# Performance work log

Measured on AMD Instinct MI355X. Metric: run time of the kernel, lower is better.

## Reference

```python
import jax, jax.numpy as jnp
import numpy as np

B, S, D, H = 1, 2048, 768, 12
E, K, I = 8, 2, 1024          # routed experts, top-k, expert inter dim
IS = 2 * I                    # shared-expert inter dim (n_shared_experts * moe_inter_dim)
EPS = 1e-5
ROUTE_SCALE = 1.0


def rmsnorm(x, w, eps=EPS):
    xf = x.astype(jnp.float32)
    return (xf * jax.lax.rsqrt(jnp.mean(xf * xf, axis=-1, keepdims=True) + eps)).astype(x.dtype) * w


def setup_inputs() -> dict:
    key = jax.random.key(0)
    ks = jax.random.split(key, 8)
    sc = 0.02
    return {
        "x": jax.random.normal(ks[0], (B, S, D), jnp.float32),
        "norm1_w": jnp.ones((D,), jnp.float32),
        "norm3_w": jnp.ones((D,), jnp.float32),
        "gate_w": jax.random.normal(ks[1], (E, D), jnp.float32) * sc,
        "w1": jax.random.normal(ks[2], (E, I, D), jnp.float32) * sc,
        "b1": jnp.zeros((E, I), jnp.float32),
        "w2": jax.random.normal(ks[3], (E, D, I), jnp.float32) * sc,
        "b2": jnp.zeros((E, D), jnp.float32),
        "w3": jax.random.normal(ks[4], (E, I, D), jnp.float32) * sc,
        "b3": jnp.zeros((E, I), jnp.float32),
        "fc1_w": jax.random.normal(ks[5], (IS, D), jnp.float32) * sc,
        "fc1_b": jnp.zeros((IS,), jnp.float32),
        "fc2_w": jax.random.normal(ks[6], (D, IS), jnp.float32) * sc,
        "fc2_b": jnp.zeros((D,), jnp.float32),
    }


def _forward(x, norm1_w, norm3_w, gate_w, w1, b1, w2, b2, w3, b3,
             fc1_w, fc1_b, fc2_w, fc2_b):
    b, s, d = x.shape
    hd = d // H

    # ---- self-attention (no qkv/out projections in the original module) ----
    xn = rmsnorm(x, norm1_w)
    qkv = xn.reshape(b, s, H, hd).transpose(0, 2, 1, 3)      # [b,h,s,hd]
    scores = jnp.einsum("bhqd,bhkd->bhqk", qkv, qkv) / np.sqrt(hd)
    attn = jax.nn.softmax(scores, axis=-1)
    ao = jnp.einsum("bhqk,bhkd->bhqd", attn, qkv)
    attn_out = ao.transpose(0, 2, 1, 3).reshape(b, s, d)
    out = x + attn_out

    # ---- MoE on norm3(out) ----
    xf = rmsnorm(out, norm3_w).reshape(-1, d)                # [N, D]
    n = xf.shape[0]

    # Gate: softmax scoring, n_groups=1 (no group masking), no bias (dim != 7168)
    logits = xf @ gate_w.T                                    # [N, E]
    sc = jax.nn.softmax(logits.astype(jnp.float32), axis=-1)  # max-subtract folded in
    _, idx = jax.lax.top_k(sc, K)                             # [N, K]
    weights = jnp.take_along_axis(sc, idx, axis=-1)
    weights = jnp.clip(weights, 1e-7) * ROUTE_SCALE
    weights = weights.astype(xf.dtype)

    # combine matrix: per-token dense expert weights (zeros for unselected)
    cmb = jnp.zeros((n, E), xf.dtype).at[jnp.arange(n)[:, None], idx].add(weights)

    # SwiGLU experts, batched over E (zero combine weight == not dispatched)
    a = jnp.einsum("nd,eid->nei", xf, w1) + b1                # [N,E,I]
    g = jnp.einsum("nd,eid->nei", xf, w3) + b3
    h = jax.nn.silu(a) * g
    eo = jnp.einsum("nei,edi->ned", h, w2) + b2               # [N,E,D]
    y = jnp.einsum("ned,ne->nd", eo, cmb)

    # shared experts (SiLU MLP)
    z = jax.nn.silu(xf @ fc1_w.T + fc1_b) @ fc2_w.T + fc2_b

    moe_out = (y + z).reshape(b, s, d)
    return out + moe_out


def reference(x, norm1_w, norm3_w, gate_w, w1, b1, w2, b2, w3, b3,
              fc1_w, fc1_b, fc2_w, fc2_b):
    return _forward(x, norm1_w, norm3_w, gate_w, w1, b1, w2, b2, w3, b3,
                    fc1_w, fc1_b, fc2_w, fc2_b)
```

## Files before the change

### kernel.cpp

```cpp
#include <hip/hip_runtime.h>
#include <math.h>

#define SEQ    2048
#define DMODEL 768
#define NHEAD  12
#define NEXP   8
#define IDIM   1024
#define ISH    2048
#define KVS    4
#define NE2    10
#define ATTN_BLOCKS 1536
#define CVT_BLOCKS 10752

typedef unsigned short u16;
typedef short s16x8 __attribute__((ext_vector_type(8)));
typedef u16   u16x8 __attribute__((ext_vector_type(8)));
typedef float f32x4 __attribute__((ext_vector_type(4)));

#define MFMA_BF16(a, b, c) __builtin_amdgcn_mfma_f32_16x16x32_bf16((a), (b), (c), 0, 0, 0)

__device__ __forceinline__ void glds16(const void* g, void* l) {
  __builtin_amdgcn_global_load_lds(
      (const __attribute__((address_space(1))) unsigned int*)g,
      (__attribute__((address_space(3))) unsigned int*)l, 16, 0, 0);
}

__device__ __forceinline__ u16 f2b(float f) {
  unsigned int u = __float_as_uint(f);
  unsigned int r = u + 0x7fffu + ((u >> 16) & 1u);
  return (u16)(r >> 16);
}
__device__ __forceinline__ float b2f(u16 v) {
  return __uint_as_float(((unsigned int)v) << 16);
}

__global__ __launch_bounds__(256) void rmsnorm_kernel(const float* __restrict__ x,
                                                      const float* __restrict__ n1w,
                                                      u16* __restrict__ xnb,
                                                      int* __restrict__ counts) {
  const int tid = threadIdx.x;
  if (blockIdx.x == 0 && tid < 16) counts[tid] = 0;
  const int row = blockIdx.x;
  const float* r = x + (size_t)row * DMODEL;
  float v0 = r[tid], v1 = r[tid + 256], v2 = r[tid + 512];
  float ss = v0 * v0 + v1 * v1 + v2 * v2;
  __shared__ float red[256];
  red[tid] = ss;
  __syncthreads();
  for (int s = 128; s > 0; s >>= 1) {
    if (tid < s) red[tid] += red[tid + s];
    __syncthreads();
  }
  float rms = rsqrtf(red[0] * (1.f / DMODEL) + 1e-5f);
  u16* ob = xnb + (size_t)row * DMODEL;
  ob[tid]       = f2b(v0 * rms * n1w[tid]);
  ob[tid + 256] = f2b(v1 * rms * n1w[tid + 256]);
  ob[tid + 512] = f2b(v2 * rms * n1w[tid + 512]);
}

__global__ __launch_bounds__(256) void attn_cvt_kernel(
    const u16* __restrict__ xnb, u16* __restrict__ Opart,
    float* __restrict__ Mpart, float* __restrict__ Lpart,
    const float* __restrict__ w1, const float* __restrict__ w3, const float* __restrict__ w2,
    const float* __restrict__ fc1, const float* __restrict__ fc2,
    u16* __restrict__ w1b, u16* __restrict__ w3b, u16* __restrict__ w2b,
    u16* __restrict__ fc1b, u16* __restrict__ fc2b) {
  const int tid = threadIdx.x;
  if (blockIdx.x >= ATTN_BLOCKS) {
    long i = (long)(blockIdx.x - ATTN_BLOCKS) * 256 + tid;
    const long NW8 = (long)NEXP * IDIM * DMODEL / 8;
    const long NF8 = (long)ISH * DMODEL / 8;
    const float* s; u16* d; long o;
    if      (i < NW8)             { s = w1;  d = w1b;  o = i; }
    else if (i < 2 * NW8)         { s = w3;  d = w3b;  o = i - NW8; }
    else if (i < 3 * NW8)         { s = w2;  d = w2b;  o = i - 2 * NW8; }
    else if (i < 3 * NW8 + NF8)   { s = fc1; d = fc1b; o = i - 3 * NW8; }
    else                          { s = fc2; d = fc2b; o = i - 3 * NW8 - NF8; }
    float4 a = ((const float4*)s)[2 * o], b = ((const float4*)s)[2 * o + 1];
    u16x8 v;
    v[0] = f2b(a.x); v[1] = f2b(a.y); v[2] = f2b(a.z); v[3] = f2b(a.w);
    v[4] = f2b(b.x); v[5] = f2b(b.y); v[6] = f2b(b.z); v[7] = f2b(b.w);
    ((u16x8*)d)[o] = v;
    return;
  }
  __shared__ u16 Qs[64][72];
  __shared__ u16 Ks[64][72];
  __shared__ u16 Vt[64][72];
  __shared__ u16 Ps[64][72];
  const int q0 = (blockIdx.x & 31) * 64;
  const int h = (blockIdx.x >> 5) % NHEAD;
  const int kvs = blockIdx.x / (32 * NHEAD);
  const int lane = tid & 63, w = tid >> 6;
  const int quad = lane >> 4, l15 = lane & 15;
  const size_t hoff = (size_t)h * 64;

  for (int cc = tid; cc < 512; cc += 256) {
    int row = cc >> 3, col8 = (cc & 7) * 8;
    *(u16x8*)&Qs[row][col8] = *(const u16x8*)(xnb + (size_t)(q0 + row) * DMODEL + hoff + col8);
  }
  __syncthreads();
  const s16x8 aq0 = *(const s16x8*)&Qs[16 * w + l15][quad * 8];
  const s16x8 aq1 = *(const s16x8*)&Qs[16 * w + l15][32 + quad * 8];

  f32x4 o[4] = {};
  float mrow[4], lrow[4];
#pragma unroll
  for (int r = 0; r < 4; r++) { mrow[r] = -INFINITY; lrow[r] = 0.f; }

  const int it0 = kvs * (SEQ / 64 / KVS);
  for (int it = 0; it < SEQ / 64 / KVS; it++) {
    const int k0 = (it0 + it) * 64;
    for (int cc = tid; cc < 512; cc += 256) {
      int row = cc >> 3, col8 = (cc & 7) * 8;
      *(u16x8*)&Ks[row][col8] = *(const u16x8*)(xnb + (size_t)(k0 + row) * DMODEL + hoff + col8);
    }
    __syncthreads();

    {
      const int rp = tid & 31, dc = ((tid >> 5) & 7) * 8;
      u16x8 v0 = *(const u16x8*)&Ks[2 * rp][dc];
      u16x8 v1 = *(const u16x8*)&Ks[2 * rp + 1][dc];
#pragma unroll
      for (int j = 0; j < 8; j++) {
        *(unsigned int*)&Vt[dc + j][2 * rp] =
            (unsigned int)v0[j] | ((unsigned int)v1[j] << 16);
      }
    }

    f32x4 s4[4] = {};
#pragma unroll
    for (int jt = 0; jt < 4; jt++) {
      s16x8 b0 = *(const s16x8*)&Ks[16 * jt + l15][quad * 8];
      s16x8 b1 = *(const s16x8*)&Ks[16 * jt + l15][32 + quad * 8];
      s4[jt] = MFMA_BF16(aq0, b0, s4[jt]);
      s4[jt] = MFMA_BF16(aq1, b1, s4[jt]);
      s4[jt] *= 0.125f;
    }

#pragma unroll
    for (int r = 0; r < 4; r++) {
      float mx = mrow[r];
#pragma unroll
      for (int jt = 0; jt < 4; jt++) mx = fmaxf(mx, s4[jt][r]);
#pragma unroll
      for (int m = 1; m <= 8; m <<= 1) mx = fmaxf(mx, __shfl_xor(mx, m, 64));
      float al = __expf(mrow[r] - mx);
      mrow[r] = mx;
      float pv[4], sum = 0.f;
#pragma unroll
      for (int jt = 0; jt < 4; jt++) { pv[jt] = __expf(s4[jt][r] - mx); sum += pv[jt]; }
#pragma unroll
      for (int m = 1; m <= 8; m <<= 1) sum += __shfl_xor(sum, m, 64);
      lrow[r] = lrow[r] * al + sum;
#pragma unroll
      for (int jt = 0; jt < 4; jt++) o[jt][r] *= al;
#pragma unroll
      for (int jt = 0; jt < 4; jt++) Ps[16 * w + quad * 4 + r][16 * jt + l15] = f2b(pv[jt]);
    }
    __syncthreads();

    s16x8 ap0 = *(const s16x8*)&Ps[16 * w + l15][quad * 8];
    s16x8 ap1 = *(const s16x8*)&Ps[16 * w + l15][32 + quad * 8];
#pragma unroll
    for (int jt = 0; jt < 4; jt++) {
      s16x8 bv0 = *(const s16x8*)&Vt[16 * jt + l15][quad * 8];
      s16x8 bv1 = *(const s16x8*)&Vt[16 * jt + l15][32 + quad * 8];
      o[jt] = MFMA_BF16(ap0, bv0, o[jt]);
      o[jt] = MFMA_BF16(ap1, bv1, o[jt]);
    }
  }

  const int hk = h * KVS + kvs;
#pragma unroll
  for (int r = 0; r < 4; r++) {
    int q = q0 + 16 * w + quad * 4 + r;
    size_t base = (size_t)q * (KVS * NHEAD) + hk;
#pragma unroll
    for (int jt = 0; jt < 4; jt++)
      Opart[base * 64 + 16 * jt + l15] = f2b(o[jt][r]);
    if (l15 == 0) {
      Mpart[base] = mrow[r];
      Lpart[base] = lrow[r];
    }
  }
}

__global__ __launch_bounds__(256) void fused_post_kernel(
    const u16* __restrict__ Opart, const float* __restrict__ Mpart,
    const float* __restrict__ Lpart, const float* __restrict__ x,
    const float* __restrict__ n3w, const float* __restrict__ gw,
    u16* __restrict__ xfb, float* __restrict__ out,
    int* __restrict__ counts, int* __restrict__ toklist, float* __restrict__ wtlist) {
  const int t = blockIdx.x;
  const int tid = threadIdx.x;
  const int lane = tid & 63, w = tid >> 6;
  __shared__ u16 Os[48 * 64];
  __shared__ float MsLs[96];
  __shared__ float ssP[4];
  __shared__ float geP[4][NEXP];

  const u16* orow = Opart + (size_t)t * (48 * 64);
  for (int c = tid; c < 384; c += 256)
    *(u16x8*)&Os[c * 8] = *(const u16x8*)&orow[c * 8];
  if (tid < 96)
    MsLs[tid] = (tid < 48) ? Mpart[(size_t)t * 48 + tid]
                           : Lpart[(size_t)t * 48 + (tid - 48)];
  __syncthreads();

  float val[3];
  float ss = 0.f;
  const float* xr = x + (size_t)t * DMODEL;
  float* outr = out + (size_t)t * DMODEL;
#pragma unroll
  for (int j = 0; j < 3; j++) {
    const int ii = 3 * w + j;
    float m0 = MsLs[ii * 4 + 0], m1 = MsLs[ii * 4 + 1];
    float m2 = MsLs[ii * 4 + 2], m3 = MsLs[ii * 4 + 3];
    float mh = fmaxf(fmaxf(m0, m1), fmaxf(m2, m3));
    float c0 = __expf(m0 - mh), c1 = __expf(m1 - mh);
    float c2 = __expf(m2 - mh), c3 = __expf(m3 - mh);
    float Lh = c0 * MsLs[48 + ii * 4 + 0] + c1 * MsLs[48 + ii * 4 + 1] +
               c2 * MsLs[48 + ii * 4 + 2] + c3 * MsLs[48 + ii * 4 + 3];
    float O = c0 * b2f(Os[(ii * 4 + 0) * 64 + lane]) +
              c1 * b2f(Os[(ii * 4 + 1) * 64 + lane]) +
              c2 * b2f(Os[(ii * 4 + 2) * 64 + lane]) +
              c3 * b2f(Os[(ii * 4 + 3) * 64 + lane]);
    float v = xr[ii * 64 + lane] + O / Lh;
    outr[ii * 64 + lane] = v;
    val[j] = v;
    ss += v * v;
  }
#pragma unroll
  for (int off = 32; off >= 1; off >>= 1) ss += __shfl_xor(ss, off, 64);
  if (lane == 0) ssP[w] = ss;
  __syncthreads();
  float rms = rsqrtf((ssP[0] + ssP[1] + ssP[2] + ssP[3]) * (1.f / DMODEL) + 1e-5f);

  float ge[NEXP] = {};
#pragma unroll
  for (int j = 0; j < 3; j++) {
    int c = (3 * w + j) * 64 + lane;
    float xn = val[j] * rms * n3w[c];
    xfb[(size_t)t * DMODEL + c] = f2b(xn);
#pragma unroll
    for (int e = 0; e < NEXP; e++) ge[e] = fmaf(xn, gw[e * DMODEL + c], ge[e]);
  }
#pragma unroll
  for (int off = 32; off >= 1; off >>= 1)
#pragma unroll
    for (int e = 0; e < NEXP; e++) ge[e] += __shfl_xor(ge[e], off, 64);
  if (lane == 0)
#pragma unroll
    for (int e = 0; e < NEXP; e++) geP[w][e] = ge[e];
  __syncthreads();

  if (tid == 0) {
    float p[NEXP], mx = -INFINITY, s = 0.f;
#pragma unroll
    for (int e = 0; e < NEXP; e++) {
      p[e] = geP[0][e] + geP[1][e] + geP[2][e] + geP[3][e];
      mx = fmaxf(mx, p[e]);
    }
#pragma unroll
    for (int e = 0; e < NEXP; e++) { p[e] = __expf(p[e] - mx); s += p[e]; }
    int e0 = 0; float b0 = p[0];
    for (int e = 1; e < NEXP; e++) if (p[e] > b0) { b0 = p[e]; e0 = e; }
    int e1 = -1; float b1v = -1.f;
    for (int e = 0; e < NEXP; e++) if (e != e0 && p[e] > b1v) { b1v = p[e]; e1 = e; }
    float inv = 1.f / s;
    int pos0 = atomicAdd(&counts[e0], 1);
    toklist[e0 * SEQ + pos0] = t;
    wtlist[e0 * SEQ + pos0] = fmaxf(b0 * inv, 1e-7f);
    int pos1 = atomicAdd(&counts[e1], 1);
    toklist[e1 * SEQ + pos1] = t;
    wtlist[e1 * SEQ + pos1] = fmaxf(b1v * inv, 1e-7f);
  }
}

__global__ __launch_bounds__(256) void gemm1_kernel(
    const u16* __restrict__ xfb,
    const u16* __restrict__ w1b, const u16* __restrict__ w3b, const u16* __restrict__ fc1b,
    const float* __restrict__ b1, const float* __restrict__ b3, const float* __restrict__ fc1_b,
    const int* __restrict__ counts, const int* __restrict__ toklist, u16* __restrict__ hb) {
  __shared__ u16 As[64][32];
  __shared__ u16 W1s[128][32];
  __shared__ u16 W3s[128][32];
  __shared__ int rIdx[64];
  const int e = blockIdx.z;
  const bool routed = (e < NEXP);
  int cnt, off;
  if (routed) {
    cnt = counts[e];
    off = 0;
    for (int i = 0; i < e; i++) off += counts[i];
  } else {
    cnt = SEQ;
    off = 2 * SEQ + (e - NEXP) * SEQ;
  }
  const int m0 = blockIdx.y * 64;
  if (m0 >= cnt) return;
  const int n0 = blockIdx.x * 128;
  const int tid = threadIdx.x;
  if (tid < 64) {
    int rr = m0 + tid;
    rIdx[tid] = routed ? toklist[e * SEQ + (rr < cnt ? rr : cnt - 1)] : rr;
  }
  __syncthreads();
  const u16* W1 = routed ? w1b + (size_t)e * IDIM * DMODEL
                         : fc1b + (size_t)(e - NEXP) * IDIM * DMODEL;
  const ptrdiff_t d31 = w3b - w1b;

  const int lane = tid & 63, w = tid >> 6;
  const int quad = lane >> 4, l15 = lane & 15;
  const int wy = w >> 1, wx = w & 1;
  const int srow = lane >> 2;
  const int schunk = ((lane & 3) ^ ((lane >> 3) & 3)) * 8;
  const int cb = (quad ^ ((l15 >> 1) & 3)) * 8;

  const u16* aS   = xfb + (size_t)rIdx[16 * w + srow] * DMODEL + schunk;
  const u16* w1S0 = W1 + (size_t)(n0 + 32 * w + srow) * DMODEL + schunk;
  const u16* w1S1 = W1 + (size_t)(n0 + 32 * w + 16 + srow) * DMODEL + schunk;

  f32x4 acc1[2][4] = {};
  f32x4 acc3[2][4] = {};
  for (int k0 = 0; k0 < DMODEL; k0 += 32) {
    glds16(aS + k0, &As[16 * w][0]);
    glds16(w1S0 + k0, &W1s[32 * w][0]);
    glds16(w1S1 + k0, &W1s[32 * w + 16][0]);
    if (routed) {
      glds16(w1S0 + d31 + k0, &W3s[32 * w][0]);
      glds16(w1S1 + d31 + k0, &W3s[32 * w + 16][0]);
    }
    __syncthreads();
    s16x8 af[2], w1f[4];
#pragma unroll
    for (int i = 0; i < 2; i++) af[i] = *(const s16x8*)&As[32 * wy + 16 * i + l15][cb];
#pragma unroll
    for (int j = 0; j < 4; j++) w1f[j] = *(const s16x8*)&W1s[64 * wx + 16 * j + l15][cb];
#pragma unroll
    for (int i = 0; i < 2; i++)
#pragma unroll
      for (int j = 0; j < 4; j++)
        acc1[i][j] = MFMA_BF16(af[i], w1f[j], acc1[i][j]);
    if (routed) {
      s16x8 w3f[4];
#pragma unroll
      for (int j = 0; j < 4; j++) w3f[j] = *(const s16x8*)&W3s[64 * wx + 16 * j + l15][cb];
#pragma unroll
      for (int i = 0; i < 2; i++)
#pragma unroll
        for (int j = 0; j < 4; j++)
          acc3[i][j] = MFMA_BF16(af[i], w3f[j], acc3[i][j]);
    }
    __syncthreads();
  }

#pragma unroll
  for (int j = 0; j < 4; j++) {
    int n = n0 + 64 * wx + 16 * j + l15;
    float b1v = routed ? b1[e * IDIM + n] : fc1_b[(e - NEXP) * IDIM + n];
    float b3v = routed ? b3[e * IDIM + n] : 0.f;
#pragma unroll
    for (int i = 0; i < 2; i++) {
#pragma unroll
      for (int r = 0; r < 4; r++) {
        int rr = m0 + 32 * wy + 16 * i + quad * 4 + r;
        if (rr < cnt) {
          float a = acc1[i][j][r] + b1v;
          float g = routed ? (acc3[i][j][r] + b3v) : 1.f;
          float hv = a / (1.f + __expf(-a)) * g;
          hb[(size_t)(off + rr) * IDIM + n] = f2b(hv);
        }
      }
    }
  }
}

__global__ __launch_bounds__(256) void gemm2_kernel(
    const u16* __restrict__ hb,
    const u16* __restrict__ w2b, const u16* __restrict__ fc2b,
    const float* __restrict__ b2, const float* __restrict__ fc2_b,
    const int* __restrict__ counts, const int* __restrict__ toklist,
    const float* __restrict__ wtlist, float* __restrict__ out) {
  __shared__ u16 As[64][32];
  __shared__ u16 Ws[128][32];
  const int n0 = blockIdx.x * 128;
  if (n0 >= DMODEL) return;
  const int e = blockIdx.z >> 2;
  const int ks = blockIdx.z & 3;
  const bool routed = (e < NEXP);
  int cnt, off;
  if (routed) {
    cnt = counts[e];
    off = 0;
    for (int i = 0; i < e; i++) off += counts[i];
  } else {
    cnt = SEQ;
    off = 2 * SEQ + (e - NEXP) * SEQ;
  }
  const int m0 = blockIdx.y * 64;
  if (m0 >= cnt) return;
  const int tid = threadIdx.x;

  const u16* Wb; int ldw, kof;
  if (routed) { Wb = w2b + (size_t)e * DMODEL * IDIM; ldw = IDIM; kof = 0; }
  else        { Wb = fc2b;                            ldw = ISH;  kof = (e - NEXP) * IDIM; }
  kof += ks * (IDIM / 4);

  const int lane = tid & 63, w = tid >> 6;
  const int quad = lane >> 4, l15 = lane & 15;
  const int wy = w >> 1, wx = w & 1;
  const int srow = lane >> 2;
  const int schunk = ((lane & 3) ^ ((lane >> 3) & 3)) * 8;
  const int cb = (quad ^ ((l15 >> 1) & 3)) * 8;

  int ra = m0 + 16 * w + srow;
  ra = off + (ra < cnt ? ra : cnt - 1);
  const u16* aS  = hb + (size_t)ra * IDIM + ks * (IDIM / 4) + schunk;
  const u16* wS0 = Wb + (size_t)(n0 + 32 * w + srow) * ldw + kof + schunk;
  const u16* wS1 = Wb + (size_t)(n0 + 32 * w + 16 + srow) * ldw + kof + schunk;

  f32x4 acc[2][4] = {};
  for (int k0 = 0; k0 < IDIM / 4; k0 += 32) {
    glds16(aS + k0, &As[16 * w][0]);
    glds16(wS0 + k0, &Ws[32 * w][0]);
    glds16(wS1 + k0, &Ws[32 * w + 16][0]);
    __syncthreads();
    s16x8 af[2], wf[4];
#pragma unroll
    for (int i = 0; i < 2; i++) af[i] = *(const s16x8*)&As[32 * wy + 16 * i + l15][cb];
#pragma unroll
    for (int j = 0; j < 4; j++) wf[j] = *(const s16x8*)&Ws[64 * wx + 16 * j + l15][cb];
#pragma unroll
    for (int i = 0; i < 2; i++)
#pragma unroll
      for (int j = 0; j < 4; j++)
        acc[i][j] = MFMA_BF16(af[i], wf[j], acc[i][j]);
    __syncthreads();
  }

#pragma unroll
  for (int j = 0; j < 4; j++) {
    int n = n0 + 64 * wx + 16 * j + l15;
    float bv = 0.f;
    if (ks == 0) bv = routed ? b2[e * DMODEL + n] : (e == NEXP ? fc2_b[n] : 0.f);
#pragma unroll
    for (int i = 0; i < 2; i++) {
#pragma unroll
      for (int r = 0; r < 4; r++) {
        int rr = m0 + 32 * wy + 16 * i + quad * 4 + r;
        if (rr < cnt) {
          int tok; float wt;
          if (routed) { tok = toklist[e * SEQ + rr]; wt = wtlist[e * SEQ + rr]; }
          else        { tok = rr;                    wt = 1.f; }
          atomicAdd(&out[(size_t)tok * DMODEL + n], wt * (acc[i][j][r] + bv));
        }
      }
    }
  }
}

extern "C" void kernel_launch(void* const* d_in, const int* in_sizes, int n_in,
                              void* d_out, int out_size, void* d_ws, size_t ws_size,
                              hipStream_t stream) {
  const float* x       = (const float*)d_in[0];
  const float* norm1_w = (const float*)d_in[1];
  const float* norm3_w = (const float*)d_in[2];
  const float* gate_w  = (const float*)d_in[3];
  const float* w1      = (const float*)d_in[4];
  const float* b1      = (const float*)d_in[5];
  const float* w2      = (const float*)d_in[6];
  const float* b2      = (const float*)d_in[7];
  const float* w3      = (const float*)d_in[8];
  const float* b3      = (const float*)d_in[9];
  const float* fc1_w   = (const float*)d_in[10];
  const float* fc1_b   = (const float*)d_in[11];
  const float* fc2_w   = (const float*)d_in[12];
  const float* fc2_b   = (const float*)d_in[13];
  float* out = (float*)d_out;

  char* p = (char*)d_ws;
  u16*   xnb    = (u16*)p;   p += (size_t)SEQ * DMODEL * 2;
  u16*   xfb    = (u16*)p;   p += (size_t)SEQ * DMODEL * 2;
  u16*   hb     = (u16*)p;   p += (size_t)4 * SEQ * IDIM * 2;
  u16*   Opart  = (u16*)p;   p += (size_t)KVS * NHEAD * SEQ * 64 * 2;
  float* Mpart  = (float*)p; p += (size_t)KVS * NHEAD * SEQ * 4;
  float* Lpart  = (float*)p; p += (size_t)KVS * NHEAD * SEQ * 4;
  u16*   w1b    = (u16*)p;   p += (size_t)NEXP * IDIM * DMODEL * 2;
  u16*   w3b    = (u16*)p;   p += (size_t)NEXP * IDIM * DMODEL * 2;
  u16*   w2b    = (u16*)p;   p += (size_t)NEXP * DMODEL * IDIM * 2;
  u16*   fc1b   = (u16*)p;   p += (size_t)ISH * DMODEL * 2;
  u16*   fc2b   = (u16*)p;   p += (size_t)DMODEL * ISH * 2;
  int*   counts = (int*)p;   p += 256;
  int*   toklist= (int*)p;   p += (size_t)NEXP * SEQ * 4;
  float* wtlist = (float*)p; p += (size_t)NEXP * SEQ * 4;

  rmsnorm_kernel<<<SEQ, 256, 0, stream>>>(x, norm1_w, xnb, counts);
  attn_cvt_kernel<<<ATTN_BLOCKS + CVT_BLOCKS, 256, 0, stream>>>(
      xnb, Opart, Mpart, Lpart, w1, w3, w2, fc1_w, fc2_w,
      w1b, w3b, w2b, fc1b, fc2b);
  fused_post_kernel<<<SEQ, 256, 0, stream>>>(Opart, Mpart, Lpart, x, norm3_w, gate_w,
                                             xfb, out, counts, toklist, wtlist);
  gemm1_kernel<<<dim3(IDIM / 128, SEQ / 64, NE2), 256, 0, stream>>>(
      xfb, w1b, w3b, fc1b, b1, b3, fc1_b, counts, toklist, hb);
  gemm2_kernel<<<dim3(8, SEQ / 64, NE2 * 4), 256, 0, stream>>>(
      hb, w2b, fc2b, b2, fc2_b, counts, toklist, wtlist, out);
  (void)in_sizes; (void)n_in; (void)out_size; (void)ws_size;
}
```

Baseline: 378.8 us.

## Widen GEMM K-tiles to 64, shrink gemm1 N-tile, drop gemm2 split-K

Both MoE GEMMs now stage 64-wide K slices in shared memory with a new XOR swizzle, which halves the number of sync barriers per K. gemm1 moves from 128 to 64 output columns per block, doubling its grid for more parallelism. gemm2 drops its 4-way split-K, so each output tile runs the full K and issues a quarter of the atomic adds. The trade-off is fewer blocks and longer serial K loops in gemm2, plus more redundant activation loads in gemm1.

```diff
diff --git a/kernel.cpp b/kernel.cpp
--- a/kernel.cpp
+++ b/kernel.cpp
@@ -282,9 +282,9 @@
     const u16* __restrict__ w1b, const u16* __restrict__ w3b, const u16* __restrict__ fc1b,
     const float* __restrict__ b1, const float* __restrict__ b3, const float* __restrict__ fc1_b,
     const int* __restrict__ counts, const int* __restrict__ toklist, u16* __restrict__ hb) {
-  __shared__ u16 As[64][32];
-  __shared__ u16 W1s[128][32];
-  __shared__ u16 W3s[128][32];
+  __shared__ u16 As[64][64];
+  __shared__ u16 W1s[64][64];
+  __shared__ u16 W3s[64][64];
   __shared__ int rIdx[64];
   const int e = blockIdx.z;
   const bool routed = (e < NEXP);
@@ -299,7 +299,7 @@
   }
   const int m0 = blockIdx.y * 64;
   if (m0 >= cnt) return;
-  const int n0 = blockIdx.x * 128;
+  const int n0 = blockIdx.x * 64;
   const int tid = threadIdx.x;
   if (tid < 64) {
     int rr = m0 + tid;
@@ -313,51 +313,59 @@
   const int lane = tid & 63, w = tid >> 6;
   const int quad = lane >> 4, l15 = lane & 15;
   const int wy = w >> 1, wx = w & 1;
-  const int srow = lane >> 2;
-  const int schunk = ((lane & 3) ^ ((lane >> 3) & 3)) * 8;
-  const int cb = (quad ^ ((l15 >> 1) & 3)) * 8;
-
-  const u16* aS   = xfb + (size_t)rIdx[16 * w + srow] * DMODEL + schunk;
-  const u16* w1S0 = W1 + (size_t)(n0 + 32 * w + srow) * DMODEL + schunk;
-  const u16* w1S1 = W1 + (size_t)(n0 + 32 * w + 16 + srow) * DMODEL + schunk;
-
-  f32x4 acc1[2][4] = {};
-  f32x4 acc3[2][4] = {};
-  for (int k0 = 0; k0 < DMODEL; k0 += 32) {
-    glds16(aS + k0, &As[16 * w][0]);
-    glds16(w1S0 + k0, &W1s[32 * w][0]);
-    glds16(w1S1 + k0, &W1s[32 * w + 16][0]);
+  const int lr8 = lane >> 3;
+  const int sch = ((lane & 7) ^ lr8) * 8;
+
+  const u16 *aS[2], *w1S[2];
+#pragma unroll
+  for (int c = 0; c < 2; c++) {
+    int tr = 16 * w + 8 * c + lr8;
+    aS[c]  = xfb + (size_t)rIdx[tr] * DMODEL + sch;
+    w1S[c] = W1 + (size_t)(n0 + tr) * DMODEL + sch;
+  }
+
+  f32x4 acc1[2][2] = {};
+  f32x4 acc3[2][2] = {};
+  for (int k0 = 0; k0 < DMODEL; k0 += 64) {
+#pragma unroll
+    for (int c = 0; c < 2; c++) glds16(aS[c] + k0, &As[16 * w + 8 * c][0]);
+#pragma unroll
+    for (int c = 0; c < 2; c++) glds16(w1S[c] + k0, &W1s[16 * w + 8 * c][0]);
     if (routed) {
-      glds16(w1S0 + d31 + k0, &W3s[32 * w][0]);
-      glds16(w1S1 + d31 + k0, &W3s[32 * w + 16][0]);
-    }
-    __syncthreads();
-    s16x8 af[2], w1f[4];
-#pragma unroll
-    for (int i = 0; i < 2; i++) af[i] = *(const s16x8*)&As[32 * wy + 16 * i + l15][cb];
-#pragma unroll
-    for (int j = 0; j < 4; j++) w1f[j] = *(const s16x8*)&W1s[64 * wx + 16 * j + l15][cb];
-#pragma unroll
-    for (int i = 0; i < 2; i++)
-#pragma unroll
-      for (int j = 0; j < 4; j++)
-        acc1[i][j] = MFMA_BF16(af[i], w1f[j], acc1[i][j]);
-    if (routed) {
-      s16x8 w3f[4];
-#pragma unroll
-      for (int j = 0; j < 4; j++) w3f[j] = *(const s16x8*)&W3s[64 * wx + 16 * j + l15][cb];
+#pragma unroll
+      for (int c = 0; c < 2; c++) glds16(w1S[c] + d31 + k0, &W3s[16 * w + 8 * c][0]);
+    }
+    __syncthreads();
+#pragma unroll
+    for (int kk = 0; kk < 2; kk++) {
+      const int cb = (((kk * 4 + quad) ^ (l15 & 7))) * 8;
+      s16x8 af[2], w1f[2];
+#pragma unroll
+      for (int i = 0; i < 2; i++) af[i] = *(const s16x8*)&As[32 * wy + 16 * i + l15][cb];
+#pragma unroll
+      for (int j = 0; j < 2; j++) w1f[j] = *(const s16x8*)&W1s[32 * wx + 16 * j + l15][cb];
 #pragma unroll
       for (int i = 0; i < 2; i++)
 #pragma unroll
-        for (int j = 0; j < 4; j++)
-          acc3[i][j] = MFMA_BF16(af[i], w3f[j], acc3[i][j]);
-    }
-    __syncthreads();
-  }
-
-#pragma unroll
-  for (int j = 0; j < 4; j++) {
-    int n = n0 + 64 * wx + 16 * j + l15;
+        for (int j = 0; j < 2; j++)
+          acc1[i][j] = MFMA_BF16(af[i], w1f[j], acc1[i][j]);
+      if (routed) {
+        s16x8 w3f[2];
+#pragma unroll
+        for (int j = 0; j < 2; j++) w3f[j] = *(const s16x8*)&W3s[32 * wx + 16 * j + l15][cb];
+#pragma unroll
+        for (int i = 0; i < 2; i++)
+#pragma unroll
+          for (int j = 0; j < 2; j++)
+            acc3[i][j] = MFMA_BF16(af[i], w3f[j], acc3[i][j]);
+      }
+    }
+    __syncthreads();
+  }
+
+#pragma unroll
+  for (int j = 0; j < 2; j++) {
+    int n = n0 + 32 * wx + 16 * j + l15;
     float b1v = routed ? b1[e * IDIM + n] : fc1_b[(e - NEXP) * IDIM + n];
     float b3v = routed ? b3[e * IDIM + n] : 0.f;
 #pragma unroll
@@ -382,12 +390,11 @@
     const float* __restrict__ b2, const float* __restrict__ fc2_b,
     const int* __restrict__ counts, const int* __restrict__ toklist,
     const float* __restrict__ wtlist, float* __restrict__ out) {
-  __shared__ u16 As[64][32];
-  __shared__ u16 Ws[128][32];
+  __shared__ u16 As[64][64];
+  __shared__ u16 Ws[128][64];
   const int n0 = blockIdx.x * 128;
   if (n0 >= DMODEL) return;
-  const int e = blockIdx.z >> 2;
-  const int ks = blockIdx.z & 3;
+  const int e = blockIdx.z;
   const bool routed = (e < NEXP);
   int cnt, off;
   if (routed) {
@@ -405,45 +412,55 @@
   const u16* Wb; int ldw, kof;
   if (routed) { Wb = w2b + (size_t)e * DMODEL * IDIM; ldw = IDIM; kof = 0; }
   else        { Wb = fc2b;                            ldw = ISH;  kof = (e - NEXP) * IDIM; }
-  kof += ks * (IDIM / 4);
 
   const int lane = tid & 63, w = tid >> 6;
   const int quad = lane >> 4, l15 = lane & 15;
   const int wy = w >> 1, wx = w & 1;
-  const int srow = lane >> 2;
-  const int schunk = ((lane & 3) ^ ((lane >> 3) & 3)) * 8;
-  const int cb = (quad ^ ((l15 >> 1) & 3)) * 8;
-
-  int ra = m0 + 16 * w + srow;
-  ra = off + (ra < cnt ? ra : cnt - 1);
-  const u16* aS  = hb + (size_t)ra * IDIM + ks * (IDIM / 4) + schunk;
-  const u16* wS0 = Wb + (size_t)(n0 + 32 * w + srow) * ldw + kof + schunk;
-  const u16* wS1 = Wb + (size_t)(n0 + 32 * w + 16 + srow) * ldw + kof + schunk;
+  const int lr8 = lane >> 3;
+  const int sch = ((lane & 7) ^ lr8) * 8;
+
+  const u16* aS[2];
+#pragma unroll
+  for (int c = 0; c < 2; c++) {
+    int ra = m0 + 16 * w + 8 * c + lr8;
+    ra = off + (ra < cnt ? ra : cnt - 1);
+    aS[c] = hb + (size_t)ra * IDIM + sch;
+  }
+  const u16* wS[4];
+#pragma unroll
+  for (int c = 0; c < 4; c++) {
+    int nr = n0 + 32 * w + 8 * c + lr8;
+    wS[c] = Wb + (size_t)nr * ldw + kof + sch;
+  }
 
   f32x4 acc[2][4] = {};
-  for (int k0 = 0; k0 < IDIM / 4; k0 += 32) {
-    glds16(aS + k0, &As[16 * w][0]);
-    glds16(wS0 + k0, &Ws[32 * w][0]);
-    glds16(wS1 + k0, &Ws[32 * w + 16][0]);
-    __syncthreads();
-    s16x8 af[2], wf[4];
-#pragma unroll
-    for (int i = 0; i < 2; i++) af[i] = *(const s16x8*)&As[32 * wy + 16 * i + l15][cb];
-#pragma unroll
-    for (int j = 0; j < 4; j++) wf[j] = *(const s16x8*)&Ws[64 * wx + 16 * j + l15][cb];
-#pragma unroll
-    for (int i = 0; i < 2; i++)
-#pragma unroll
-      for (int j = 0; j < 4; j++)
-        acc[i][j] = MFMA_BF16(af[i], wf[j], acc[i][j]);
+  for (int k0 = 0; k0 < IDIM; k0 += 64) {
+#pragma unroll
+    for (int c = 0; c < 2; c++) glds16(aS[c] + k0, &As[16 * w + 8 * c][0]);
+#pragma unroll
+    for (int c = 0; c < 4; c++) glds16(wS[c] + k0, &Ws[32 * w + 8 * c][0]);
+    __syncthreads();
+#pragma unroll
+    for (int kk = 0; kk < 2; kk++) {
+      const int cb = (((kk * 4 + quad) ^ (l15 & 7))) * 8;
+      s16x8 af[2], wf[4];
+#pragma unroll
+      for (int i = 0; i < 2; i++) af[i] = *(const s16x8*)&As[32 * wy + 16 * i + l15][cb];
+#pragma unroll
+      for (int j = 0; j < 4; j++) wf[j] = *(const s16x8*)&Ws[64 * wx + 16 * j + l15][cb];
+#pragma unroll
+      for (int i = 0; i < 2; i++)
+#pragma unroll
+        for (int j = 0; j < 4; j++)
+          acc[i][j] = MFMA_BF16(af[i], wf[j], acc[i][j]);
+    }
     __syncthreads();
   }
 
 #pragma unroll
   for (int j = 0; j < 4; j++) {
     int n = n0 + 64 * wx + 16 * j + l15;
-    float bv = 0.f;
-    if (ks == 0) bv = routed ? b2[e * DMODEL + n] : (e == NEXP ? fc2_b[n] : 0.f);
+    float bv = routed ? b2[e * DMODEL + n] : (e == NEXP ? fc2_b[n] : 0.f);
 #pragma unroll
     for (int i = 0; i < 2; i++) {
 #pragma unroll
@@ -501,9 +518,9 @@
       w1b, w3b, w2b, fc1b, fc2b);
   fused_post_kernel<<<SEQ, 256, 0, stream>>>(Opart, Mpart, Lpart, x, norm3_w, gate_w,
                                              xfb, out, counts, toklist, wtlist);
-  gemm1_kernel<<<dim3(IDIM / 128, SEQ / 64, NE2), 256, 0, stream>>>(
+  gemm1_kernel<<<dim3(IDIM / 64, SEQ / 64, NE2), 256, 0, stream>>>(
       xfb, w1b, w3b, fc1b, b1, b3, fc1_b, counts, toklist, hb);
-  gemm2_kernel<<<dim3(8, SEQ / 64, NE2 * 4), 256, 0, stream>>>(
+  gemm2_kernel<<<dim3(8, SEQ / 64, NE2), 256, 0, stream>>>(
       hb, w2b, fc2b, b2, fc2_b, counts, toklist, wtlist, out);
   (void)in_sizes; (void)n_in; (void)out_size; (void)ws_size;
 }
```

Result: faster. 324.9 us (-14.2%).
